# Optimization experiments

Hardware: AMD Instinct MI355X
Metric: run time of the kernel (lower is better)

Reference implementation:

```python
import jax, jax.numpy as jnp
import numpy as np

BETA = 0.5
N = 4096

def setup_inputs() -> dict:
    key = jax.random.key(0)
    k1, k2, k3 = jax.random.split(key, 3)
    A = jax.random.uniform(k1, (N, N), dtype=jnp.float32)
    h = jax.random.normal(k2, (N, N), dtype=jnp.float32)
    W = jax.random.normal(k3, (N, N), dtype=jnp.float32) * (1.0 / np.sqrt(N))
    return {"A": A, "h": h, "W": W}

def reference(A, h, W):
    # degrees from original A (before self-loops); D = diag(deg) + I is diagonal,
    # so torch.inverse(D) == elementwise reciprocal 1/(deg+1)
    deg = jnp.sum(A, axis=1)                       # [N]
    inv_d = 1.0 / (deg + 1.0)                      # [N]
    A_I = A + jnp.eye(A.shape[0], dtype=A.dtype)   # A += I
    # A_st = (A+I) @ diag(inv_d): scale columns
    A_st = A_I * inv_d[None, :]                    # [N,N]
    # A_st_11 = A_st @ h is dead code in the original (never used) -> skipped
    temp = BETA * h + (1.0 - BETA) * A_st          # [N,N]
    return temp @ W                                # [N,N]
```

## Files before the change

### kernel.cpp

```cpp
#include <hip/hip_runtime.h>
#include <hip/hip_bf16.h>

typedef unsigned short u16;
typedef unsigned int u32;
typedef __attribute__((ext_vector_type(8))) short bf16x8;
typedef __attribute__((ext_vector_type(4))) short s16x4;
typedef __attribute__((ext_vector_type(4))) float f32x4;

#define NN 4096

__device__ __forceinline__ u16 f2bf(float f) {
    union { float f; u32 u; } v; v.f = f;
    u32 r = v.u + 0x7fffu + ((v.u >> 16) & 1u);
    return (u16)(r >> 16);
}

__global__ void rowsum_kernel(const float* __restrict__ A, float* __restrict__ invd) {
    const int row = blockIdx.x;
    const float4* a4 = reinterpret_cast<const float4*>(A + (size_t)row * NN);
    float s = 0.f;
    #pragma unroll
    for (int i = 0; i < 4; ++i) {
        float4 v = a4[threadIdx.x + i * 256];
        s += v.x + v.y + v.z + v.w;
    }
    #pragma unroll
    for (int off = 32; off > 0; off >>= 1) s += __shfl_down(s, off, 64);
    __shared__ float ws[4];
    if ((threadIdx.x & 63) == 0) ws[threadIdx.x >> 6] = s;
    __syncthreads();
    if (threadIdx.x == 0) {
        float t = ws[0] + ws[1] + ws[2] + ws[3];
        invd[row] = 1.0f / (t + 1.0f);
    }
}

__global__ void make_temp_kernel(const float* __restrict__ A, const float* __restrict__ h,
                                 const float* __restrict__ invd, u16* __restrict__ T) {
    const size_t g = ((size_t)blockIdx.x * 256 + threadIdx.x) * 8;
    const int row = (int)(g >> 12);
    const int col = (int)(g & 4095);
    const float4* a4 = reinterpret_cast<const float4*>(A + g);
    const float4* h4 = reinterpret_cast<const float4*>(h + g);
    const float4* d4 = reinterpret_cast<const float4*>(invd + col);
    float4 a0 = a4[0], a1 = a4[1];
    float4 h0 = h4[0], h1 = h4[1];
    float4 dd0 = d4[0], dd1 = d4[1];
    float av[8] = {a0.x,a0.y,a0.z,a0.w,a1.x,a1.y,a1.z,a1.w};
    float hv[8] = {h0.x,h0.y,h0.z,h0.w,h1.x,h1.y,h1.z,h1.w};
    float dv[8] = {dd0.x,dd0.y,dd0.z,dd0.w,dd1.x,dd1.y,dd1.z,dd1.w};
    bf16x8 o;
    #pragma unroll
    for (int j = 0; j < 8; ++j) {
        float aa = av[j] + ((col + j == row) ? 1.0f : 0.0f);
        float t = 0.5f * hv[j] + 0.5f * aa * dv[j];
        o[j] = (short)f2bf(t);
    }
    *reinterpret_cast<bf16x8*>(T + g) = o;
}

__global__ void transposeW_kernel(const float* __restrict__ W, u16* __restrict__ Wt) {
    __shared__ float tile[64][65];
    const int nt = blockIdx.x & 63;
    const int kt = blockIdx.x >> 6;
    const int k0 = kt * 64, n0 = nt * 64;
    const int tr = threadIdx.x >> 4;
    const int tc = (threadIdx.x & 15) * 4;
    #pragma unroll
    for (int rr = 0; rr < 64; rr += 16) {
        float4 v = *reinterpret_cast<const float4*>(&W[(size_t)(k0 + tr + rr) * NN + n0 + tc]);
        tile[tr + rr][tc + 0] = v.x;
        tile[tr + rr][tc + 1] = v.y;
        tile[tr + rr][tc + 2] = v.z;
        tile[tr + rr][tc + 3] = v.w;
    }
    __syncthreads();
    #pragma unroll
    for (int rr = 0; rr < 64; rr += 16) {
        const int n = tr + rr;
        s16x4 o;
        #pragma unroll
        for (int j = 0; j < 4; ++j) o[j] = (short)f2bf(tile[tc + j][n]);
        *reinterpret_cast<s16x4*>(&Wt[(size_t)(n0 + n) * NN + k0 + tc]) = o;
    }
}


#define GLD16(g, l) __builtin_amdgcn_global_load_lds( \
    (const __attribute__((address_space(1))) void*)(g), \
    (__attribute__((address_space(3))) void*)(l), 16, 0, 0)

#define SBAR()  do { __builtin_amdgcn_sched_barrier(0); \
    __builtin_amdgcn_s_barrier(); asm volatile("" ::: "memory"); } while (0)
#define LGKM0() do { asm volatile("s_waitcnt lgkmcnt(0)" ::: "memory"); \
    __builtin_amdgcn_sched_barrier(0); } while (0)

__global__ __launch_bounds__(512, 2) void gemm_kernel(
    const u16* __restrict__ Atl,
    const u16* __restrict__ Btl,
    float* __restrict__ C)
{
    __shared__ u16 S[2][4][8192];

    const int tid  = threadIdx.x;
    const int wid  = tid >> 6;
    const int lane = tid & 63;
    const int llo  = lane & 15;
    const int lhi  = lane >> 4;
    const int wr   = wid >> 2;
    const int wc   = wid & 3;

    const int swz = ((int)blockIdx.x & 7) * 32 + ((int)blockIdx.x >> 3);
    const int bm = swz >> 4, bn = swz & 15;
    const int tileRow = bm * 256, tileCol = bn * 256;

    const int r0 = tid >> 3;
    const int kc = (((tid & 7) ^ (r0 & 7)) << 3);
    const size_t R64  = (size_t)64 * NN;
    const size_t R128 = (size_t)128 * NN;
    const u16* gA = Atl + (size_t)(tileRow + r0) * NN + kc;
    const u16* gB = Btl + (size_t)(tileCol + r0) * NN + kc;

    #define STG(PTR, DSTBASE) do { \
        GLD16((PTR),       (DSTBASE) + tid * 8); \
        GLD16((PTR) + R64, (DSTBASE) + 4096 + tid * 8); } while (0)

    int offA[8], offB[4];
    #pragma unroll
    for (int m = 0; m < 8; ++m) {
        const int row = m * 16 + llo;
        offA[m] = row * 64 + ((lhi ^ (row & 7)) << 3);
    }
    #pragma unroll
    for (int n = 0; n < 4; ++n) {
        const int row = (wc & 1) * 64 + n * 16 + llo;
        offB[n] = row * 64 + ((lhi ^ (row & 7)) << 3);
    }

    f32x4 acc[8][4];
    #pragma unroll
    for (int m = 0; m < 8; ++m)
        #pragma unroll
        for (int n = 0; n < 4; ++n)
            acc[m][n] = (f32x4){0.f, 0.f, 0.f, 0.f};

    {
        u16* b0p = (u16*)&S[0][0][0];
        u16* b1p = (u16*)&S[1][0][0];
        STG(gA,              b0p + 0 * 8192);
        STG(gA + R128,       b0p + 1 * 8192);
        STG(gB,              b0p + 2 * 8192);
        STG(gB + R128,       b0p + 3 * 8192);
        STG(gA + 64,         b1p + 0 * 8192);
        STG(gA + R128 + 64,  b1p + 1 * 8192);
        STG(gB + 64,         b1p + 2 * 8192);
        STG(gB + R128 + 64,  b1p + 3 * 8192);
    }
    asm volatile("s_waitcnt vmcnt(8)" ::: "memory");
    __builtin_amdgcn_s_barrier();
    asm volatile("" ::: "memory");

    #pragma unroll 1
    for (int g = 0; g < 64; ++g) {
        u16* cb = (u16*)&S[g & 1][0][0];
        const u16* sAr = cb + wr * 8192;
        const u16* sBr = cb + (2 + (wc >> 1)) * 8192;
        const int koff = (g + 2) * 64;
        const bool stg = g <= 61;

        bf16x8 a0[4][2], a1[4][2], b0[2][2], b1[2][2];

        #pragma unroll
        for (int m = 0; m < 4; ++m) {
            a0[m][0] = *reinterpret_cast<const bf16x8*>(sAr + offA[m]);
            a0[m][1] = *reinterpret_cast<const bf16x8*>(sAr + (offA[m] ^ 32));
        }
        #pragma unroll
        for (int n = 0; n < 2; ++n) {
            b0[n][0] = *reinterpret_cast<const bf16x8*>(sBr + offB[n]);
            b0[n][1] = *reinterpret_cast<const bf16x8*>(sBr + (offB[n] ^ 32));
        }
        asm volatile("s_waitcnt lgkmcnt(8)" ::: "memory");
        SBAR();
        LGKM0();
        __builtin_amdgcn_s_setprio(1);
        #pragma unroll
        for (int ks = 0; ks < 2; ++ks)
            #pragma unroll
            for (int m = 0; m < 4; ++m)
                #pragma unroll
                for (int n = 0; n < 2; ++n)
                    acc[m][n] = __builtin_amdgcn_mfma_f32_16x16x32_bf16(a0[m][ks], b0[n][ks], acc[m][n], 0, 0, 0);
        __builtin_amdgcn_s_setprio(0);
        SBAR();

        #pragma unroll
        for (int n = 0; n < 2; ++n) {
            b1[n][0] = *reinterpret_cast<const bf16x8*>(sBr + offB[2 + n]);
            b1[n][1] = *reinterpret_cast<const bf16x8*>(sBr + (offB[2 + n] ^ 32));
        }
        SBAR();
        LGKM0();
        __builtin_amdgcn_s_setprio(1);
        #pragma unroll
        for (int ks = 0; ks < 2; ++ks)
            #pragma unroll
            for (int m = 0; m < 4; ++m)
                #pragma unroll
                for (int n = 0; n < 2; ++n)
                    acc[m][2 + n] = __builtin_amdgcn_mfma_f32_16x16x32_bf16(a0[m][ks], b1[n][ks], acc[m][2 + n], 0, 0, 0);
        __builtin_amdgcn_s_setprio(0);
        SBAR();

        #pragma unroll
        for (int m = 0; m < 4; ++m) {
            a1[m][0] = *reinterpret_cast<const bf16x8*>(sAr + offA[4 + m]);
            a1[m][1] = *reinterpret_cast<const bf16x8*>(sAr + (offA[4 + m] ^ 32));
        }
        if (stg) {
            STG(gB + koff,        cb + 2 * 8192);
            STG(gB + R128 + koff, cb + 3 * 8192);
        }
        SBAR();
        LGKM0();
        __builtin_amdgcn_s_setprio(1);
        #pragma unroll
        for (int ks = 0; ks < 2; ++ks)
            #pragma unroll
            for (int m = 0; m < 4; ++m)
                #pragma unroll
                for (int n = 0; n < 2; ++n)
                    acc[4 + m][n] = __builtin_amdgcn_mfma_f32_16x16x32_bf16(a1[m][ks], b0[n][ks], acc[4 + m][n], 0, 0, 0);
        __builtin_amdgcn_s_setprio(0);
        SBAR();

        if (stg) {
            STG(gA + koff,        cb + 0 * 8192);
            STG(gA + R128 + koff, cb + 1 * 8192);
        }
        if (g <= 61)      asm volatile("s_waitcnt vmcnt(8)" ::: "memory");
        else if (g == 62) asm volatile("s_waitcnt vmcnt(0)" ::: "memory");
        SBAR();
        __builtin_amdgcn_s_setprio(1);
        #pragma unroll
        for (int ks = 0; ks < 2; ++ks)
            #pragma unroll
            for (int m = 0; m < 4; ++m)
                #pragma unroll
                for (int n = 0; n < 2; ++n)
                    acc[4 + m][2 + n] = __builtin_amdgcn_mfma_f32_16x16x32_bf16(a1[m][ks], b1[n][ks], acc[4 + m][2 + n], 0, 0, 0);
        __builtin_amdgcn_s_setprio(0);
        if (g < 63) SBAR();
    }
    #undef STG

    #pragma unroll
    for (int m = 0; m < 8; ++m) {
        #pragma unroll
        for (int n = 0; n < 4; ++n) {
            const size_t rbase = (size_t)(tileRow + wr * 128 + m * 16 + lhi * 4) * NN
                               + tileCol + wc * 64 + n * 16 + llo;
            #pragma unroll
            for (int j = 0; j < 4; ++j)
                C[rbase + (size_t)j * NN] = acc[m][n][j];
        }
    }
}

extern "C" void kernel_launch(void* const* d_in, const int* in_sizes, int n_in,
                              void* d_out, int out_size, void* d_ws, size_t ws_size,
                              hipStream_t stream) {
    const float* A = (const float*)d_in[0];
    const float* h = (const float*)d_in[1];
    const float* W = (const float*)d_in[2];
    float* out = (float*)d_out;

    float* invd = (float*)d_ws;
    u16* temp = (u16*)((char*)d_ws + 16384);
    u16* wt   = temp + (size_t)NN * NN;

    rowsum_kernel<<<NN, 256, 0, stream>>>(A, invd);
    make_temp_kernel<<<(NN * (size_t)NN) / (256 * 8), 256, 0, stream>>>(A, h, invd, temp);
    transposeW_kernel<<<(NN / 64) * (NN / 64), 256, 0, stream>>>(W, wt);
    gemm_kernel<<<256, 512, 0, stream>>>(temp, wt, out);
}
```

Baseline: 178.5 us.

## Stagger GEMM tile prefetch so half of next tile streams during current compute

Restructures the double-buffered global-to-LDS prefetch schedule. Instead of issuing both halves of the tile two steps ahead, each iteration loads the second halves of A and B for the next tile into the other buffer and the first halves for the tile two ahead into the current buffer. The vmcnt waits are tightened to match. The aim is to spread global loads more evenly across the MFMA phases and reduce outstanding-load pressure, at the cost of harder-to-verify buffer-hazard ordering.

Measured after the change: 175.2 us. About the same (-1.9%).

```diff
diff --git a/kernel.cpp b/kernel.cpp
--- a/kernel.cpp
+++ b/kernel.cpp
@@ -144,29 +144,27 @@
         for (int n = 0; n < 4; ++n)
             acc[m][n] = (f32x4){0.f, 0.f, 0.f, 0.f};
 
-    {
-        u16* b0p = (u16*)&S[0][0][0];
-        u16* b1p = (u16*)&S[1][0][0];
-        STG(gA,              b0p + 0 * 8192);
-        STG(gA + R128,       b0p + 1 * 8192);
-        STG(gB,              b0p + 2 * 8192);
-        STG(gB + R128,       b0p + 3 * 8192);
-        STG(gA + 64,         b1p + 0 * 8192);
-        STG(gA + R128 + 64,  b1p + 1 * 8192);
-        STG(gB + 64,         b1p + 2 * 8192);
-        STG(gB + R128 + 64,  b1p + 3 * 8192);
-    }
-    asm volatile("s_waitcnt vmcnt(8)" ::: "memory");
+    u16* const B0p = (u16*)&S[0][0][0];
+    u16* const B1p = (u16*)&S[1][0][0];
+
+    STG(gA,             B0p + 0 * 8192);
+    STG(gA + R128,      B0p + 1 * 8192);
+    STG(gB,             B0p + 2 * 8192);
+    STG(gB + R128,      B0p + 3 * 8192);
+    STG(gA + 64,        B1p + 0 * 8192);
+    STG(gB + 64,        B1p + 2 * 8192);
+    asm volatile("s_waitcnt vmcnt(4)" ::: "memory");
     __builtin_amdgcn_s_barrier();
     asm volatile("" ::: "memory");
 
     #pragma unroll 1
     for (int g = 0; g < 64; ++g) {
-        u16* cb = (u16*)&S[g & 1][0][0];
+        u16* cb = (g & 1) ? B1p : B0p;
+        u16* nb = (g & 1) ? B0p : B1p;
         const u16* sAr = cb + wr * 8192;
         const u16* sBr = cb + (2 + (wc >> 1)) * 8192;
-        const int koff = (g + 2) * 64;
-        const bool stg = g <= 61;
+        const int k1 = (g + 1) * 64;
+        const int k2 = (g + 2) * 64;
 
         bf16x8 a0[4][2], a1[4][2], b0[2][2], b1[2][2];
 
@@ -180,6 +178,7 @@
             b0[n][0] = *reinterpret_cast<const bf16x8*>(sBr + offB[n]);
             b0[n][1] = *reinterpret_cast<const bf16x8*>(sBr + (offB[n] ^ 32));
         }
+        if (g <= 62) STG(gA + R128 + k1, nb + 1 * 8192);
         asm volatile("s_waitcnt lgkmcnt(8)" ::: "memory");
         SBAR();
         LGKM0();
@@ -199,6 +198,7 @@
             b1[n][0] = *reinterpret_cast<const bf16x8*>(sBr + offB[2 + n]);
             b1[n][1] = *reinterpret_cast<const bf16x8*>(sBr + (offB[2 + n] ^ 32));
         }
+        if (g <= 62) STG(gB + R128 + k1, nb + 3 * 8192);
         SBAR();
         LGKM0();
         __builtin_amdgcn_s_setprio(1);
@@ -217,10 +217,7 @@
             a1[m][0] = *reinterpret_cast<const bf16x8*>(sAr + offA[4 + m]);
             a1[m][1] = *reinterpret_cast<const bf16x8*>(sAr + (offA[4 + m] ^ 32));
         }
-        if (stg) {
-            STG(gB + koff,        cb + 2 * 8192);
-            STG(gB + R128 + koff, cb + 3 * 8192);
-        }
+        if (g <= 61) STG(gB + k2, cb + 2 * 8192);
         SBAR();
         LGKM0();
         __builtin_amdgcn_s_setprio(1);
@@ -234,11 +231,8 @@
         __builtin_amdgcn_s_setprio(0);
         SBAR();
 
-        if (stg) {
-            STG(gA + koff,        cb + 0 * 8192);
-            STG(gA + R128 + koff, cb + 1 * 8192);
-        }
-        if (g <= 61)      asm volatile("s_waitcnt vmcnt(8)" ::: "memory");
+        if (g <= 61) STG(gA + k2, cb + 0 * 8192);
+        if (g <= 61)      asm volatile("s_waitcnt vmcnt(4)" ::: "memory");
         else if (g == 62) asm volatile("s_waitcnt vmcnt(0)" ::: "memory");
         SBAR();
         __builtin_amdgcn_s_setprio(1);
```
